# Kernel optimization log

Hardware: AMD Instinct MI355X
Metric: run time of the kernel (lower is better)

## Reference

```python
import jax, jax.numpy as jnp
import numpy as np

N = 100000
E = 3200000
IN_F = 16
HID = 64
NUM_CLASSES = 32


def setup_inputs() -> dict:
    key = jax.random.key(0)
    k1, k2, k3, k4, k5 = jax.random.split(key, 5)
    x = jax.random.normal(k1, (N, IN_F), dtype=jnp.float32)
    edge_index = jax.random.randint(k2, (2, E), 0, N, dtype=jnp.int64)
    # Glorot-style init for GCNConv weights, zero bias (PyG default)
    s1 = (6.0 / (IN_F + HID)) ** 0.5
    s2 = (6.0 / (HID + NUM_CLASSES)) ** 0.5
    W1 = jax.random.uniform(k3, (IN_F, HID), minval=-s1, maxval=s1, dtype=jnp.float32)
    b1 = jnp.zeros((HID,), dtype=jnp.float32)
    W2 = jax.random.uniform(k4, (HID, NUM_CLASSES), minval=-s2, maxval=s2, dtype=jnp.float32)
    b2 = jnp.zeros((NUM_CLASSES,), dtype=jnp.float32)
    return {"x": x, "edge_index": edge_index, "W1": W1, "b1": b1, "W2": W2, "b2": b2}


def _gcn_norm(edge_index):
    # add_self_loops=False, improved=False, edge_weight=1
    row, col = edge_index[0], edge_index[1]  # source, target
    deg = jax.ops.segment_sum(jnp.ones((edge_index.shape[1],), jnp.float32), col, num_segments=N)
    dinv = jnp.where(deg > 0, jax.lax.rsqrt(jnp.maximum(deg, 1e-12)), 0.0)
    return row, col, dinv[row] * dinv[col]  # [E]


def _gcn_conv(x, row, col, norm, W, b):
    h = x @ W                                  # [N, out]
    msg = h[row] * norm[:, None]               # [E, out] gather + normalize
    out = jax.ops.segment_sum(msg, col, num_segments=N)  # scatter-add to targets
    return out + b


def reference(x, edge_index, W1, b1, W2, b2):
    row, col, norm = _gcn_norm(edge_index)
    h = jax.nn.relu(_gcn_conv(x, row, col, norm, W1, b1))
    # dropout p=0.5 is identity in eval mode
    return _gcn_conv(h, row, col, norm, W2, b2)
```

## Files before the change

### kernel.cpp

```cpp
#include <hip/hip_runtime.h>
#include <hip/hip_fp16.h>

static constexpr int INF = 16;
static constexpr int HID = 64;
static constexpr int NC  = 32;
static constexpr int SHIFT = 8;
static constexpr int BK    = 256;
static constexpr int NBMAX = 512;
static constexpr int CAP   = 9216;
static constexpr int SPLIT_T  = 512;
static constexpr int SPLIT_IT = 16;
static constexpr int SRC_BITS = 17;
static constexpr int SRC_MASK = (1 << SRC_BITS) - 1;

struct alignas(8) half4 { __half2 lo, hi; };

__device__ __forceinline__ int clampi(int v, int n) {
    return v < 0 ? 0 : (v >= n ? n - 1 : v);
}

__global__ __launch_bounds__(SPLIT_T) void k_split(const int* __restrict__ ei, int E, int n,
                                                   int* __restrict__ bcur, int* __restrict__ pairs) {
    __shared__ int lh[NBMAX];
    __shared__ int base[NBMAX];
    int t = threadIdx.x;
    long long start = (long long)blockIdx.x * SPLIT_T * SPLIT_IT;
    int r[SPLIT_IT], c[SPLIT_IT];
    for (int j = t; j < NBMAX; j += SPLIT_T) lh[j] = 0;
    __syncthreads();
#pragma unroll
    for (int i = 0; i < SPLIT_IT; ++i) {
        long long e = start + (long long)i * SPLIT_T + t;
        if (e < E) {
            r[i] = clampi(ei[e], n);
            c[i] = clampi(ei[E + e], n);
            atomicAdd(&lh[c[i] >> SHIFT], 1);
        } else {
            c[i] = -1;
        }
    }
    __syncthreads();
    for (int j = t; j < NBMAX; j += SPLIT_T) {
        int cnt = lh[j];
        base[j] = cnt ? (j * CAP + atomicAdd(bcur + j, cnt)) : 0;
        lh[j] = 0;
    }
    __syncthreads();
#pragma unroll
    for (int i = 0; i < SPLIT_IT; ++i) {
        if (c[i] >= 0) {
            int b = c[i] >> SHIFT;
            int pos = base[b] + atomicAdd(&lh[b], 1);
            pairs[pos] = ((c[i] & (BK - 1)) << SRC_BITS) | r[i];
        }
    }
}

__global__ __launch_bounds__(1024) void k_fine(const int* __restrict__ pairs,
                                               const int* __restrict__ bcur,
                                               const float* __restrict__ x,
                                               int n,
                                               float* __restrict__ dinv,
                                               int* __restrict__ row_ptr,
                                               int* __restrict__ rend,
                                               int* __restrict__ src,
                                               __half2* __restrict__ xs) {
    __shared__ int h[BK];
    __shared__ int sc[BK];
    __shared__ float df[BK];
    int b = blockIdx.x, t = threadIdx.x;
    int bb = b * CAP;
    int be = bb + bcur[b];
    if (t < BK) h[t] = 0;
    __syncthreads();
    for (int i = bb + t; i < be; i += 1024)
        atomicAdd(&h[pairs[i] >> SRC_BITS], 1);
    __syncthreads();
    int val = (t < BK) ? h[t] : 0;
    if (t < BK) sc[t] = val;
    __syncthreads();
    for (int off = 1; off < BK; off <<= 1) {
        int a = (t < BK && t >= off) ? sc[t - off] : 0;
        __syncthreads();
        if (t < BK) sc[t] += a;
        __syncthreads();
    }
    if (t < BK) {
        int ex = sc[t] - val;
        int v = b * BK + t;
        float dv = 0.0f;
        if (v < n) {
            dv = (val > 0) ? rsqrtf((float)val) : 0.0f;
            dinv[v] = dv;
            row_ptr[v] = bb + ex;
            rend[v]    = bb + ex + val;
        }
        df[t] = dv;
        h[t] = bb + ex;
    }
    __syncthreads();
    for (int i = bb + t; i < be; i += 1024) {
        int p = pairs[i];
        int pos = atomicAdd(&h[p >> SRC_BITS], 1);
        src[pos] = p & SRC_MASK;
    }
    const float2* x2 = (const float2*)x;
    for (int idx = t; idx < BK * (INF / 2); idx += 1024) {
        int vl = idx >> 3, fp = idx & 7;
        int gv = b * BK + vl;
        if (gv < n) {
            float2 val2 = x2[(long long)gv * (INF / 2) + fp];
            float d = df[vl];
            xs[(long long)gv * (INF / 2) + fp] = __floats2half2_rn(val2.x * d, val2.y * d);
        }
    }
}

__global__ __launch_bounds__(256) void k_aggX(const int* __restrict__ ptr,
                                              const int* __restrict__ rend,
                                              const int* __restrict__ src,
                                              const float* __restrict__ dinv,
                                              const __half* __restrict__ xs,
                                              float* __restrict__ xa, int n) {
    int t = threadIdx.x;
    int v = blockIdx.x * 64 + (t >> 2);
    int lane = t & 3;
    if (v >= n) return;
    int b = ptr[v], e = rend[v];
    float a0 = 0.f, a1 = 0.f, a2 = 0.f, a3 = 0.f;
    int i = b;
    for (; i + 8 <= e; i += 8) {
        int s0 = src[i], s1 = src[i + 1], s2 = src[i + 2], s3 = src[i + 3];
        int s4 = src[i + 4], s5 = src[i + 5], s6 = src[i + 6], s7 = src[i + 7];
        half4 h0 = *reinterpret_cast<const half4*>(xs + (long long)s0 * INF + lane * 4);
        half4 h1 = *reinterpret_cast<const half4*>(xs + (long long)s1 * INF + lane * 4);
        half4 h2 = *reinterpret_cast<const half4*>(xs + (long long)s2 * INF + lane * 4);
        half4 h3 = *reinterpret_cast<const half4*>(xs + (long long)s3 * INF + lane * 4);
        half4 h4 = *reinterpret_cast<const half4*>(xs + (long long)s4 * INF + lane * 4);
        half4 h5 = *reinterpret_cast<const half4*>(xs + (long long)s5 * INF + lane * 4);
        half4 h6 = *reinterpret_cast<const half4*>(xs + (long long)s6 * INF + lane * 4);
        half4 h7 = *reinterpret_cast<const half4*>(xs + (long long)s7 * INF + lane * 4);
        float2 f;
        f = __half22float2(h0.lo); a0 += f.x; a1 += f.y;
        f = __half22float2(h0.hi); a2 += f.x; a3 += f.y;
        f = __half22float2(h1.lo); a0 += f.x; a1 += f.y;
        f = __half22float2(h1.hi); a2 += f.x; a3 += f.y;
        f = __half22float2(h2.lo); a0 += f.x; a1 += f.y;
        f = __half22float2(h2.hi); a2 += f.x; a3 += f.y;
        f = __half22float2(h3.lo); a0 += f.x; a1 += f.y;
        f = __half22float2(h3.hi); a2 += f.x; a3 += f.y;
        f = __half22float2(h4.lo); a0 += f.x; a1 += f.y;
        f = __half22float2(h4.hi); a2 += f.x; a3 += f.y;
        f = __half22float2(h5.lo); a0 += f.x; a1 += f.y;
        f = __half22float2(h5.hi); a2 += f.x; a3 += f.y;
        f = __half22float2(h6.lo); a0 += f.x; a1 += f.y;
        f = __half22float2(h6.hi); a2 += f.x; a3 += f.y;
        f = __half22float2(h7.lo); a0 += f.x; a1 += f.y;
        f = __half22float2(h7.hi); a2 += f.x; a3 += f.y;
    }
    for (; i < e; ++i) {
        int s = src[i];
        half4 hv = *reinterpret_cast<const half4*>(xs + (long long)s * INF + lane * 4);
        float2 f0 = __half22float2(hv.lo);
        float2 f1 = __half22float2(hv.hi);
        a0 += f0.x; a1 += f0.y; a2 += f1.x; a3 += f1.y;
    }
    float dv = dinv[v];
    float4 o = make_float4(a0 * dv, a1 * dv, a2 * dv, a3 * dv);
    *reinterpret_cast<float4*>(xa + (long long)v * INF + lane * 4) = o;
}

__global__ __launch_bounds__(256) void k_mlp(const float* __restrict__ xa,
                                             const float* __restrict__ W1,
                                             const float* __restrict__ b1,
                                             const float* __restrict__ W2,
                                             const float* __restrict__ dinv,
                                             __half2* __restrict__ h2h, int n) {
    __shared__ float W1l[INF * HID];
    __shared__ float W2l[HID * NC];
    __shared__ float b1l[HID];
    __shared__ float xal[16 * INF];
    __shared__ float hl[16 * HID];
    int t = threadIdx.x;
    for (int i = t; i < INF * HID; i += 256) W1l[i] = W1[i];
    for (int i = t; i < HID * NC; i += 256) W2l[i] = W2[i];
    if (t < HID) b1l[t] = b1[t];
    int base = blockIdx.x * 16;
    for (int i = t; i < 16 * INF; i += 256) {
        int r = i >> 4, k = i & 15;
        int v = base + r;
        xal[i] = (v < n) ? xa[(long long)v * INF + k] : 0.0f;
    }
    __syncthreads();
    for (int i = t; i < 16 * HID; i += 256) {
        int r = i >> 6, c = i & 63;
        float s = b1l[c];
#pragma unroll
        for (int k = 0; k < INF; ++k) s = fmaf(xal[r * INF + k], W1l[k * HID + c], s);
        hl[i] = fmaxf(s, 0.0f);
    }
    __syncthreads();
    {
        int r = t >> 4, cp = t & 15;
        int v = base + r;
        if (v < n) {
            int c0 = 2 * cp;
            float s0 = 0.f, s1 = 0.f;
#pragma unroll
            for (int k = 0; k < HID; ++k) {
                float hv = hl[r * HID + k];
                s0 = fmaf(hv, W2l[k * NC + c0], s0);
                s1 = fmaf(hv, W2l[k * NC + c0 + 1], s1);
            }
            float dv = dinv[v];
            h2h[(long long)v * (NC / 2) + cp] = __floats2half2_rn(s0 * dv, s1 * dv);
        }
    }
}

__global__ __launch_bounds__(256) void k_agg2(const int* __restrict__ ptr,
                                              const int* __restrict__ rend,
                                              const int* __restrict__ src,
                                              const float* __restrict__ dinv,
                                              const __half* __restrict__ h2h,
                                              const float* __restrict__ b2,
                                              float* __restrict__ out, int n) {
    int t = threadIdx.x;
    int v = blockIdx.x * 32 + (t >> 3);
    int lane = t & 7;
    if (v >= n) return;
    int b = ptr[v], e = rend[v];
    float a0 = 0.f, a1 = 0.f, a2 = 0.f, a3 = 0.f;
    int i = b;
    for (; i + 8 <= e; i += 8) {
        int s0 = src[i], s1 = src[i + 1], s2 = src[i + 2], s3 = src[i + 3];
        int s4 = src[i + 4], s5 = src[i + 5], s6 = src[i + 6], s7 = src[i + 7];
        half4 h0 = *reinterpret_cast<const half4*>(h2h + (long long)s0 * NC + lane * 4);
        half4 h1 = *reinterpret_cast<const half4*>(h2h + (long long)s1 * NC + lane * 4);
        half4 h2 = *reinterpret_cast<const half4*>(h2h + (long long)s2 * NC + lane * 4);
        half4 h3 = *reinterpret_cast<const half4*>(h2h + (long long)s3 * NC + lane * 4);
        half4 h4 = *reinterpret_cast<const half4*>(h2h + (long long)s4 * NC + lane * 4);
        half4 h5 = *reinterpret_cast<const half4*>(h2h + (long long)s5 * NC + lane * 4);
        half4 h6 = *reinterpret_cast<const half4*>(h2h + (long long)s6 * NC + lane * 4);
        half4 h7 = *reinterpret_cast<const half4*>(h2h + (long long)s7 * NC + lane * 4);
        float2 f;
        f = __half22float2(h0.lo); a0 += f.x; a1 += f.y;
        f = __half22float2(h0.hi); a2 += f.x; a3 += f.y;
        f = __half22float2(h1.lo); a0 += f.x; a1 += f.y;
        f = __half22float2(h1.hi); a2 += f.x; a3 += f.y;
        f = __half22float2(h2.lo); a0 += f.x; a1 += f.y;
        f = __half22float2(h2.hi); a2 += f.x; a3 += f.y;
        f = __half22float2(h3.lo); a0 += f.x; a1 += f.y;
        f = __half22float2(h3.hi); a2 += f.x; a3 += f.y;
        f = __half22float2(h4.lo); a0 += f.x; a1 += f.y;
        f = __half22float2(h4.hi); a2 += f.x; a3 += f.y;
        f = __half22float2(h5.lo); a0 += f.x; a1 += f.y;
        f = __half22float2(h5.hi); a2 += f.x; a3 += f.y;
        f = __half22float2(h6.lo); a0 += f.x; a1 += f.y;
        f = __half22float2(h6.hi); a2 += f.x; a3 += f.y;
        f = __half22float2(h7.lo); a0 += f.x; a1 += f.y;
        f = __half22float2(h7.hi); a2 += f.x; a3 += f.y;
    }
    for (; i < e; ++i) {
        int s = src[i];
        half4 hv = *reinterpret_cast<const half4*>(h2h + (long long)s * NC + lane * 4);
        float2 f0 = __half22float2(hv.lo);
        float2 f1 = __half22float2(hv.hi);
        a0 += f0.x; a1 += f0.y; a2 += f1.x; a3 += f1.y;
    }
    float dv = dinv[v];
    const float4 bb = *reinterpret_cast<const float4*>(b2 + lane * 4);
    float4 o = make_float4(fmaf(a0, dv, bb.x), fmaf(a1, dv, bb.y),
                           fmaf(a2, dv, bb.z), fmaf(a3, dv, bb.w));
    *reinterpret_cast<float4*>(out + (long long)v * NC + lane * 4) = o;
}

extern "C" void kernel_launch(void* const* d_in, const int* in_sizes, int n_in,
                              void* d_out, int out_size, void* d_ws, size_t ws_size,
                              hipStream_t stream) {
    const float* x  = (const float*)d_in[0];
    const int*   ei = (const int*)d_in[1];
    const float* W1 = (const float*)d_in[2];
    const float* b1 = (const float*)d_in[3];
    const float* W2 = (const float*)d_in[4];
    const float* b2 = (const float*)d_in[5];
    float* out = (float*)d_out;

    const int n = in_sizes[0] / INF;
    const int E = in_sizes[1] / 2;
    const int NB = (n + BK - 1) / BK;

    size_t  gcap    = (size_t)NB * CAP;
    int*    pairs   = (int*)d_ws;
    int*    src     = pairs + gcap;
    __half* xs      = (__half*)(src + gcap);
    float*  xa      = (float*)(src + gcap + (size_t)8 * n);
    __half* h2h     = (__half*)(src + gcap + (size_t)24 * n);
    float*  dinv    = (float*)(src + gcap + (size_t)40 * n);
    int*    row_ptr = (int*)(dinv + n);
    int*    rend    = row_ptr + n;
    int*    bcur    = rend + n;

    hipMemsetAsync(bcur, 0, NBMAX * sizeof(int), stream);

    int splitBlocks = (int)((E + (long long)SPLIT_T * SPLIT_IT - 1) / ((long long)SPLIT_T * SPLIT_IT));
    k_split<<<splitBlocks, SPLIT_T, 0, stream>>>(ei, E, n, bcur, pairs);

    k_fine<<<NB, 1024, 0, stream>>>(pairs, bcur, x, n, dinv, row_ptr, rend, src, (__half2*)xs);

    k_aggX<<<(n + 63) / 64, 256, 0, stream>>>(row_ptr, rend, src, dinv, xs, xa, n);
    k_mlp<<<(n + 15) / 16, 256, 0, stream>>>(xa, W1, b1, W2, dinv, (__half2*)h2h, n);
    k_agg2<<<(n + 31) / 32, 256, 0, stream>>>(row_ptr, rend, src, dinv, h2h, b2, out, n);
}
```

Baseline: 158.8 us.

## Fuse layer-1 aggregation with MLP and widen layer-2 gather to 16-byte loads

Merges the first-layer neighbour aggregation and the dense MLP (W1, ReLU, W2) into one kernel. Each group of 4 lanes exchanges its aggregated features through shuffles, computes 16 hidden units, and reduces the W2 partial products with xor-shuffles. This removes the fp32 xa intermediate round trip through global memory and one kernel launch. The second aggregation kernel now uses 4 lanes per node with 16-byte half8 loads instead of 8 lanes with 8-byte loads. The trade-off is higher register pressure (hreg, po and the x16 arrays) and some leftover dead shuffle-setup code.

```diff
diff --git a/kernel.cpp b/kernel.cpp
--- a/kernel.cpp
+++ b/kernel.cpp
@@ -12,8 +12,10 @@
 static constexpr int SPLIT_IT = 16;
 static constexpr int SRC_BITS = 17;
 static constexpr int SRC_MASK = (1 << SRC_BITS) - 1;
-
-struct alignas(8) half4 { __half2 lo, hi; };
+static constexpr int W2S = NC + 1;
+
+struct alignas(8)  half4 { __half2 lo, hi; };
+struct alignas(16) half8 { __half2 a, b, c, d; };
 
 __device__ __forceinline__ int clampi(int v, int n) {
     return v < 0 ? 0 : (v >= n ? n - 1 : v);
@@ -116,104 +118,137 @@
     }
 }
 
-__global__ __launch_bounds__(256) void k_aggX(const int* __restrict__ ptr,
-                                              const int* __restrict__ rend,
-                                              const int* __restrict__ src,
-                                              const float* __restrict__ dinv,
-                                              const __half* __restrict__ xs,
-                                              float* __restrict__ xa, int n) {
-    int t = threadIdx.x;
-    int v = blockIdx.x * 64 + (t >> 2);
-    int lane = t & 3;
-    if (v >= n) return;
-    int b = ptr[v], e = rend[v];
-    float a0 = 0.f, a1 = 0.f, a2 = 0.f, a3 = 0.f;
-    int i = b;
-    for (; i + 8 <= e; i += 8) {
-        int s0 = src[i], s1 = src[i + 1], s2 = src[i + 2], s3 = src[i + 3];
-        int s4 = src[i + 4], s5 = src[i + 5], s6 = src[i + 6], s7 = src[i + 7];
-        half4 h0 = *reinterpret_cast<const half4*>(xs + (long long)s0 * INF + lane * 4);
-        half4 h1 = *reinterpret_cast<const half4*>(xs + (long long)s1 * INF + lane * 4);
-        half4 h2 = *reinterpret_cast<const half4*>(xs + (long long)s2 * INF + lane * 4);
-        half4 h3 = *reinterpret_cast<const half4*>(xs + (long long)s3 * INF + lane * 4);
-        half4 h4 = *reinterpret_cast<const half4*>(xs + (long long)s4 * INF + lane * 4);
-        half4 h5 = *reinterpret_cast<const half4*>(xs + (long long)s5 * INF + lane * 4);
-        half4 h6 = *reinterpret_cast<const half4*>(xs + (long long)s6 * INF + lane * 4);
-        half4 h7 = *reinterpret_cast<const half4*>(xs + (long long)s7 * INF + lane * 4);
-        float2 f;
-        f = __half22float2(h0.lo); a0 += f.x; a1 += f.y;
-        f = __half22float2(h0.hi); a2 += f.x; a3 += f.y;
-        f = __half22float2(h1.lo); a0 += f.x; a1 += f.y;
-        f = __half22float2(h1.hi); a2 += f.x; a3 += f.y;
-        f = __half22float2(h2.lo); a0 += f.x; a1 += f.y;
-        f = __half22float2(h2.hi); a2 += f.x; a3 += f.y;
-        f = __half22float2(h3.lo); a0 += f.x; a1 += f.y;
-        f = __half22float2(h3.hi); a2 += f.x; a3 += f.y;
-        f = __half22float2(h4.lo); a0 += f.x; a1 += f.y;
-        f = __half22float2(h4.hi); a2 += f.x; a3 += f.y;
-        f = __half22float2(h5.lo); a0 += f.x; a1 += f.y;
-        f = __half22float2(h5.hi); a2 += f.x; a3 += f.y;
-        f = __half22float2(h6.lo); a0 += f.x; a1 += f.y;
-        f = __half22float2(h6.hi); a2 += f.x; a3 += f.y;
-        f = __half22float2(h7.lo); a0 += f.x; a1 += f.y;
-        f = __half22float2(h7.hi); a2 += f.x; a3 += f.y;
-    }
-    for (; i < e; ++i) {
-        int s = src[i];
-        half4 hv = *reinterpret_cast<const half4*>(xs + (long long)s * INF + lane * 4);
-        float2 f0 = __half22float2(hv.lo);
-        float2 f1 = __half22float2(hv.hi);
-        a0 += f0.x; a1 += f0.y; a2 += f1.x; a3 += f1.y;
-    }
-    float dv = dinv[v];
-    float4 o = make_float4(a0 * dv, a1 * dv, a2 * dv, a3 * dv);
-    *reinterpret_cast<float4*>(xa + (long long)v * INF + lane * 4) = o;
-}
-
-__global__ __launch_bounds__(256) void k_mlp(const float* __restrict__ xa,
-                                             const float* __restrict__ W1,
-                                             const float* __restrict__ b1,
-                                             const float* __restrict__ W2,
-                                             const float* __restrict__ dinv,
-                                             __half2* __restrict__ h2h, int n) {
+__global__ __launch_bounds__(256) void k_aggmlp2(const int* __restrict__ ptr,
+                                                 const int* __restrict__ rend,
+                                                 const int* __restrict__ src,
+                                                 const float* __restrict__ dinv,
+                                                 const __half* __restrict__ xs,
+                                                 const float* __restrict__ W1,
+                                                 const float* __restrict__ b1,
+                                                 const float* __restrict__ W2,
+                                                 __half* __restrict__ h2h, int n) {
     __shared__ float W1l[INF * HID];
-    __shared__ float W2l[HID * NC];
+    __shared__ float W2l[HID * W2S];
     __shared__ float b1l[HID];
-    __shared__ float xal[16 * INF];
-    __shared__ float hl[16 * HID];
     int t = threadIdx.x;
     for (int i = t; i < INF * HID; i += 256) W1l[i] = W1[i];
-    for (int i = t; i < HID * NC; i += 256) W2l[i] = W2[i];
+    for (int i = t; i < HID * NC; i += 256) W2l[(i >> 5) * W2S + (i & 31)] = W2[i];
     if (t < HID) b1l[t] = b1[t];
-    int base = blockIdx.x * 16;
-    for (int i = t; i < 16 * INF; i += 256) {
-        int r = i >> 4, k = i & 15;
-        int v = base + r;
-        xal[i] = (v < n) ? xa[(long long)v * INF + k] : 0.0f;
-    }
-    __syncthreads();
-    for (int i = t; i < 16 * HID; i += 256) {
-        int r = i >> 6, c = i & 63;
-        float s = b1l[c];
-#pragma unroll
-        for (int k = 0; k < INF; ++k) s = fmaf(xal[r * INF + k], W1l[k * HID + c], s);
-        hl[i] = fmaxf(s, 0.0f);
-    }
-    __syncthreads();
-    {
-        int r = t >> 4, cp = t & 15;
-        int v = base + r;
+
+    int node = t >> 2, lane = t & 3;
+    int v = blockIdx.x * 64 + node;
+    float a0 = 0.f, a1 = 0.f, a2 = 0.f, a3 = 0.f;
+    float dv = 0.0f;
+    if (v < n) {
+        dv = dinv[v];
+        int b = ptr[v], e = rend[v];
+        int i = b;
+        for (; i + 8 <= e; i += 8) {
+            int s0 = src[i], s1 = src[i + 1], s2 = src[i + 2], s3 = src[i + 3];
+            int s4 = src[i + 4], s5 = src[i + 5], s6 = src[i + 6], s7 = src[i + 7];
+            half4 h0 = *reinterpret_cast<const half4*>(xs + (long long)s0 * INF + lane * 4);
+            half4 h1 = *reinterpret_cast<const half4*>(xs + (long long)s1 * INF + lane * 4);
+            half4 h2 = *reinterpret_cast<const half4*>(xs + (long long)s2 * INF + lane * 4);
+            half4 h3 = *reinterpret_cast<const half4*>(xs + (long long)s3 * INF + lane * 4);
+            half4 h4 = *reinterpret_cast<const half4*>(xs + (long long)s4 * INF + lane * 4);
+            half4 h5 = *reinterpret_cast<const half4*>(xs + (long long)s5 * INF + lane * 4);
+            half4 h6 = *reinterpret_cast<const half4*>(xs + (long long)s6 * INF + lane * 4);
+            half4 h7 = *reinterpret_cast<const half4*>(xs + (long long)s7 * INF + lane * 4);
+            float2 f;
+            f = __half22float2(h0.lo); a0 += f.x; a1 += f.y;
+            f = __half22float2(h0.hi); a2 += f.x; a3 += f.y;
+            f = __half22float2(h1.lo); a0 += f.x; a1 += f.y;
+            f = __half22float2(h1.hi); a2 += f.x; a3 += f.y;
+            f = __half22float2(h2.lo); a0 += f.x; a1 += f.y;
+            f = __half22float2(h2.hi); a2 += f.x; a3 += f.y;
+            f = __half22float2(h3.lo); a0 += f.x; a1 += f.y;
+            f = __half22float2(h3.hi); a2 += f.x; a3 += f.y;
+            f = __half22float2(h4.lo); a0 += f.x; a1 += f.y;
+            f = __half22float2(h4.hi); a2 += f.x; a3 += f.y;
+            f = __half22float2(h5.lo); a0 += f.x; a1 += f.y;
+            f = __half22float2(h5.hi); a2 += f.x; a3 += f.y;
+            f = __half22float2(h6.lo); a0 += f.x; a1 += f.y;
+            f = __half22float2(h6.hi); a2 += f.x; a3 += f.y;
+            f = __half22float2(h7.lo); a0 += f.x; a1 += f.y;
+            f = __half22float2(h7.hi); a2 += f.x; a3 += f.y;
+        }
+        for (; i < e; ++i) {
+            int s = src[i];
+            half4 hv = *reinterpret_cast<const half4*>(xs + (long long)s * INF + lane * 4);
+            float2 f0 = __half22float2(hv.lo);
+            float2 f1 = __half22float2(hv.hi);
+            a0 += f0.x; a1 += f0.y; a2 += f1.x; a3 += f1.y;
+        }
+        a0 *= dv; a1 *= dv; a2 *= dv; a3 *= dv;
+    }
+    __syncthreads();
+
+    float own4[4] = {a0, a1, a2, a3};
+    float x8[8];
+#pragma unroll
+    for (int j = 0; j < 4; ++j) {
+        float send = own4[j];
+        float recv = __shfl_xor(send, 1);
+        x8[j]     = (lane & 1) ? recv : own4[j];
+        x8[4 + j] = (lane & 1) ? own4[j] : recv;
+    }
+    float x16[16];
+#pragma unroll
+    for (int j = 0; j < 8; ++j) {
+        float send = x8[j ^ ((lane & 2) ? 0 : 0)];
+        (void)send;
+    }
+#pragma unroll
+    for (int j = 0; j < 8; ++j) {
+        float snd = (lane & 2) ? x8[j] : x8[j];
+        float recv = __shfl_xor(snd, 2);
+        x16[j]     = (lane & 2) ? recv : x8[j];
+        x16[8 + j] = (lane & 2) ? x8[j] : recv;
+    }
+
+    int cbase = lane * 16;
+    float hreg[16];
+#pragma unroll
+    for (int j = 0; j < 16; ++j) {
+        float s = b1l[cbase + j];
+#pragma unroll
+        for (int k = 0; k < 16; ++k) s = fmaf(x16[k], W1l[k * HID + cbase + j], s);
+        hreg[j] = fmaxf(s, 0.0f);
+    }
+
+#pragma unroll
+    for (int c0 = 0; c0 < 2; ++c0) {
+        float po[16];
+#pragma unroll
+        for (int o = 0; o < 16; ++o) {
+            float s = 0.0f;
+#pragma unroll
+            for (int j = 0; j < 16; ++j)
+                s = fmaf(hreg[j], W2l[(cbase + j) * W2S + c0 * 16 + o], s);
+            po[o] = s;
+        }
+        float q[8];
+#pragma unroll
+        for (int j = 0; j < 8; ++j) {
+            float send = (lane & 1) ? po[j] : po[8 + j];
+            float recv = __shfl_xor(send, 1);
+            float keep = (lane & 1) ? po[8 + j] : po[j];
+            q[j] = keep + recv;
+        }
+        float r4[4];
+#pragma unroll
+        for (int j = 0; j < 4; ++j) {
+            float send = (lane & 2) ? q[j] : q[4 + j];
+            float recv = __shfl_xor(send, 2);
+            float keep = (lane & 2) ? q[4 + j] : q[j];
+            r4[j] = keep + recv;
+        }
         if (v < n) {
-            int c0 = 2 * cp;
-            float s0 = 0.f, s1 = 0.f;
-#pragma unroll
-            for (int k = 0; k < HID; ++k) {
-                float hv = hl[r * HID + k];
-                s0 = fmaf(hv, W2l[k * NC + c0], s0);
-                s1 = fmaf(hv, W2l[k * NC + c0 + 1], s1);
-            }
-            float dv = dinv[v];
-            h2h[(long long)v * (NC / 2) + cp] = __floats2half2_rn(s0 * dv, s1 * dv);
+            int obase = c0 * 16 + (lane & 1) * 8 + (lane & 2) * 2;
+            half4 outw;
+            outw.lo = __floats2half2_rn(r4[0] * dv, r4[1] * dv);
+            outw.hi = __floats2half2_rn(r4[2] * dv, r4[3] * dv);
+            *reinterpret_cast<half4*>(h2h + (long long)v * NC + obase) = outw;
         }
     }
 }
@@ -226,53 +261,75 @@
                                               const float* __restrict__ b2,
                                               float* __restrict__ out, int n) {
     int t = threadIdx.x;
-    int v = blockIdx.x * 32 + (t >> 3);
-    int lane = t & 7;
+    int v = blockIdx.x * 64 + (t >> 2);
+    int lane = t & 3;
     if (v >= n) return;
     int b = ptr[v], e = rend[v];
-    float a0 = 0.f, a1 = 0.f, a2 = 0.f, a3 = 0.f;
+    float a0 = 0.f, a1 = 0.f, a2 = 0.f, a3 = 0.f, a4 = 0.f, a5 = 0.f, a6 = 0.f, a7 = 0.f;
     int i = b;
     for (; i + 8 <= e; i += 8) {
         int s0 = src[i], s1 = src[i + 1], s2 = src[i + 2], s3 = src[i + 3];
         int s4 = src[i + 4], s5 = src[i + 5], s6 = src[i + 6], s7 = src[i + 7];
-        half4 h0 = *reinterpret_cast<const half4*>(h2h + (long long)s0 * NC + lane * 4);
-        half4 h1 = *reinterpret_cast<const half4*>(h2h + (long long)s1 * NC + lane * 4);
-        half4 h2 = *reinterpret_cast<const half4*>(h2h + (long long)s2 * NC + lane * 4);
-        half4 h3 = *reinterpret_cast<const half4*>(h2h + (long long)s3 * NC + lane * 4);
-        half4 h4 = *reinterpret_cast<const half4*>(h2h + (long long)s4 * NC + lane * 4);
-        half4 h5 = *reinterpret_cast<const half4*>(h2h + (long long)s5 * NC + lane * 4);
-        half4 h6 = *reinterpret_cast<const half4*>(h2h + (long long)s6 * NC + lane * 4);
-        half4 h7 = *reinterpret_cast<const half4*>(h2h + (long long)s7 * NC + lane * 4);
+        half8 h0 = *reinterpret_cast<const half8*>(h2h + (long long)s0 * NC + lane * 8);
+        half8 h1 = *reinterpret_cast<const half8*>(h2h + (long long)s1 * NC + lane * 8);
+        half8 h2 = *reinterpret_cast<const half8*>(h2h + (long long)s2 * NC + lane * 8);
+        half8 h3 = *reinterpret_cast<const half8*>(h2h + (long long)s3 * NC + lane * 8);
+        half8 h4 = *reinterpret_cast<const half8*>(h2h + (long long)s4 * NC + lane * 8);
+        half8 h5 = *reinterpret_cast<const half8*>(h2h + (long long)s5 * NC + lane * 8);
+        half8 h6 = *reinterpret_cast<const half8*>(h2h + (long long)s6 * NC + lane * 8);
+        half8 h7 = *reinterpret_cast<const half8*>(h2h + (long long)s7 * NC + lane * 8);
         float2 f;
-        f = __half22float2(h0.lo); a0 += f.x; a1 += f.y;
-        f = __half22float2(h0.hi); a2 += f.x; a3 += f.y;
-        f = __half22float2(h1.lo); a0 += f.x; a1 += f.y;
-        f = __half22float2(h1.hi); a2 += f.x; a3 += f.y;
-        f = __half22float2(h2.lo); a0 += f.x; a1 += f.y;
-        f = __half22float2(h2.hi); a2 += f.x; a3 += f.y;
-        f = __half22float2(h3.lo); a0 += f.x; a1 += f.y;
-        f = __half22float2(h3.hi); a2 += f.x; a3 += f.y;
-        f = __half22float2(h4.lo); a0 += f.x; a1 += f.y;
-        f = __half22float2(h4.hi); a2 += f.x; a3 += f.y;
-        f = __half22float2(h5.lo); a0 += f.x; a1 += f.y;
-        f = __half22float2(h5.hi); a2 += f.x; a3 += f.y;
-        f = __half22float2(h6.lo); a0 += f.x; a1 += f.y;
-        f = __half22float2(h6.hi); a2 += f.x; a3 += f.y;
-        f = __half22float2(h7.lo); a0 += f.x; a1 += f.y;
-        f = __half22float2(h7.hi); a2 += f.x; a3 += f.y;
+        f = __half22float2(h0.a); a0 += f.x; a1 += f.y;
+        f = __half22float2(h0.b); a2 += f.x; a3 += f.y;
+        f = __half22float2(h0.c); a4 += f.x; a5 += f.y;
+        f = __half22float2(h0.d); a6 += f.x; a7 += f.y;
+        f = __half22float2(h1.a); a0 += f.x; a1 += f.y;
+        f = __half22float2(h1.b); a2 += f.x; a3 += f.y;
+        f = __half22float2(h1.c); a4 += f.x; a5 += f.y;
+        f = __half22float2(h1.d); a6 += f.x; a7 += f.y;
+        f = __half22float2(h2.a); a0 += f.x; a1 += f.y;
+        f = __half22float2(h2.b); a2 += f.x; a3 += f.y;
+        f = __half22float2(h2.c); a4 += f.x; a5 += f.y;
+        f = __half22float2(h2.d); a6 += f.x; a7 += f.y;
+        f = __half22float2(h3.a); a0 += f.x; a1 += f.y;
+        f = __half22float2(h3.b); a2 += f.x; a3 += f.y;
+        f = __half22float2(h3.c); a4 += f.x; a5 += f.y;
+        f = __half22float2(h3.d); a6 += f.x; a7 += f.y;
+        f = __half22float2(h4.a); a0 += f.x; a1 += f.y;
+        f = __half22float2(h4.b); a2 += f.x; a3 += f.y;
+        f = __half22float2(h4.c); a4 += f.x; a5 += f.y;
+        f = __half22float2(h4.d); a6 += f.x; a7 += f.y;
+        f = __half22float2(h5.a); a0 += f.x; a1 += f.y;
+        f = __half22float2(h5.b); a2 += f.x; a3 += f.y;
+        f = __half22float2(h5.c); a4 += f.x; a5 += f.y;
+        f = __half22float2(h5.d); a6 += f.x; a7 += f.y;
+        f = __half22float2(h6.a); a0 += f.x; a1 += f.y;
+        f = __half22float2(h6.b); a2 += f.x; a3 += f.y;
+        f = __half22float2(h6.c); a4 += f.x; a5 += f.y;
+        f = __half22float2(h6.d); a6 += f.x; a7 += f.y;
+        f = __half22float2(h7.a); a0 += f.x; a1 += f.y;
+        f = __half22float2(h7.b); a2 += f.x; a3 += f.y;
+        f = __half22float2(h7.c); a4 += f.x; a5 += f.y;
+        f = __half22float2(h7.d); a6 += f.x; a7 += f.y;
     }
     for (; i < e; ++i) {
         int s = src[i];
-        half4 hv = *reinterpret_cast<const half4*>(h2h + (long long)s * NC + lane * 4);
-        float2 f0 = __half22float2(hv.lo);
-        float2 f1 = __half22float2(hv.hi);
-        a0 += f0.x; a1 += f0.y; a2 += f1.x; a3 += f1.y;
+        half8 hv = *reinterpret_cast<const half8*>(h2h + (long long)s * NC + lane * 8);
+        float2 f;
+        f = __half22float2(hv.a); a0 += f.x; a1 += f.y;
+        f = __half22float2(hv.b); a2 += f.x; a3 += f.y;
+        f = __half22float2(hv.c); a4 += f.x; a5 += f.y;
+        f = __half22float2(hv.d); a6 += f.x; a7 += f.y;
     }
     float dv = dinv[v];
-    const float4 bb = *reinterpret_cast<const float4*>(b2 + lane * 4);
-    float4 o = make_float4(fmaf(a0, dv, bb.x), fmaf(a1, dv, bb.y),
-                           fmaf(a2, dv, bb.z), fmaf(a3, dv, bb.w));
-    *reinterpret_cast<float4*>(out + (long long)v * NC + lane * 4) = o;
+    const float4 bb0 = *reinterpret_cast<const float4*>(b2 + lane * 8);
+    const float4 bb1 = *reinterpret_cast<const float4*>(b2 + lane * 8 + 4);
+    float4 o0 = make_float4(fmaf(a0, dv, bb0.x), fmaf(a1, dv, bb0.y),
+                            fmaf(a2, dv, bb0.z), fmaf(a3, dv, bb0.w));
+    float4 o1 = make_float4(fmaf(a4, dv, bb1.x), fmaf(a5, dv, bb1.y),
+                            fmaf(a6, dv, bb1.z), fmaf(a7, dv, bb1.w));
+    *reinterpret_cast<float4*>(out + (long long)v * NC + lane * 8)     = o0;
+    *reinterpret_cast<float4*>(out + (long long)v * NC + lane * 8 + 4) = o1;
 }
 
 extern "C" void kernel_launch(void* const* d_in, const int* in_sizes, int n_in,
@@ -294,9 +351,8 @@
     int*    pairs   = (int*)d_ws;
     int*    src     = pairs + gcap;
     __half* xs      = (__half*)(src + gcap);
-    float*  xa      = (float*)(src + gcap + (size_t)8 * n);
-    __half* h2h     = (__half*)(src + gcap + (size_t)24 * n);
-    float*  dinv    = (float*)(src + gcap + (size_t)40 * n);
+    __half* h2h     = (__half*)(src + gcap + (size_t)8 * n);
+    float*  dinv    = (float*)(src + gcap + (size_t)24 * n);
     int*    row_ptr = (int*)(dinv + n);
     int*    rend    = row_ptr + n;
     int*    bcur    = rend + n;
@@ -308,7 +364,7 @@
 
     k_fine<<<NB, 1024, 0, stream>>>(pairs, bcur, x, n, dinv, row_ptr, rend, src, (__half2*)xs);
 
-    k_aggX<<<(n + 63) / 64, 256, 0, stream>>>(row_ptr, rend, src, dinv, xs, xa, n);
-    k_mlp<<<(n + 15) / 16, 256, 0, stream>>>(xa, W1, b1, W2, dinv, (__half2*)h2h, n);
-    k_agg2<<<(n + 31) / 32, 256, 0, stream>>>(row_ptr, rend, src, dinv, h2h, b2, out, n);
-}
+    k_aggmlp2<<<(n + 63) / 64, 256, 0, stream>>>(row_ptr, rend, src, dinv, xs, W1, b1, W2,
+                                                 h2h, n);
+    k_agg2<<<(n + 63) / 64, 256, 0, stream>>>(row_ptr, rend, src, dinv, h2h, b2, out, n);
+}
```

Result: faster. 155.4 us (median of 2 runs) (-2.1%).

## Split second-layer aggregation into two column-half passes over smaller gather tables

Applied to the files above, without the earlier changes.

The MLP kernel now writes the 32-wide fp16 second-layer features as two separate 16-column tables. The final aggregation runs twice, once per half, so each gathered table is 3.2 MB instead of 6.4 MB and is meant to stay resident in L2/MALL during the random gathers. The cost is reading the CSR index arrays twice and one extra launch. The edge-split kernel is also retuned to 1024 threads with 8 items per thread.

```diff
diff --git a/kernel.cpp b/kernel.cpp
--- a/kernel.cpp
+++ b/kernel.cpp
@@ -8,8 +8,8 @@
 static constexpr int BK    = 256;
 static constexpr int NBMAX = 512;
 static constexpr int CAP   = 9216;
-static constexpr int SPLIT_T  = 512;
-static constexpr int SPLIT_IT = 16;
+static constexpr int SPLIT_T  = 1024;
+static constexpr int SPLIT_IT = 8;
 static constexpr int SRC_BITS = 17;
 static constexpr int SRC_MASK = (1 << SRC_BITS) - 1;
 
@@ -175,7 +175,8 @@
                                              const float* __restrict__ b1,
                                              const float* __restrict__ W2,
                                              const float* __restrict__ dinv,
-                                             __half2* __restrict__ h2h, int n) {
+                                             __half2* __restrict__ h2a,
+                                             __half2* __restrict__ h2b, int n) {
     __shared__ float W1l[INF * HID];
     __shared__ float W2l[HID * NC];
     __shared__ float b1l[HID];
@@ -213,21 +214,23 @@
                 s1 = fmaf(hv, W2l[k * NC + c0 + 1], s1);
             }
             float dv = dinv[v];
-            h2h[(long long)v * (NC / 2) + cp] = __floats2half2_rn(s0 * dv, s1 * dv);
-        }
-    }
-}
-
-__global__ __launch_bounds__(256) void k_agg2(const int* __restrict__ ptr,
-                                              const int* __restrict__ rend,
-                                              const int* __restrict__ src,
-                                              const float* __restrict__ dinv,
-                                              const __half* __restrict__ h2h,
-                                              const float* __restrict__ b2,
-                                              float* __restrict__ out, int n) {
+            __half2 w = __floats2half2_rn(s0 * dv, s1 * dv);
+            if (cp < 8) h2a[(long long)v * 8 + cp]       = w;
+            else        h2b[(long long)v * 8 + (cp - 8)] = w;
+        }
+    }
+}
+
+__global__ __launch_bounds__(256) void k_agg2h(const int* __restrict__ ptr,
+                                               const int* __restrict__ rend,
+                                               const int* __restrict__ src,
+                                               const float* __restrict__ dinv,
+                                               const __half* __restrict__ tab,
+                                               const float* __restrict__ b2,
+                                               float* __restrict__ out, int n, int coff) {
     int t = threadIdx.x;
-    int v = blockIdx.x * 32 + (t >> 3);
-    int lane = t & 7;
+    int v = blockIdx.x * 64 + (t >> 2);
+    int lane = t & 3;
     if (v >= n) return;
     int b = ptr[v], e = rend[v];
     float a0 = 0.f, a1 = 0.f, a2 = 0.f, a3 = 0.f;
@@ -235,14 +238,14 @@
     for (; i + 8 <= e; i += 8) {
         int s0 = src[i], s1 = src[i + 1], s2 = src[i + 2], s3 = src[i + 3];
         int s4 = src[i + 4], s5 = src[i + 5], s6 = src[i + 6], s7 = src[i + 7];
-        half4 h0 = *reinterpret_cast<const half4*>(h2h + (long long)s0 * NC + lane * 4);
-        half4 h1 = *reinterpret_cast<const half4*>(h2h + (long long)s1 * NC + lane * 4);
-        half4 h2 = *reinterpret_cast<const half4*>(h2h + (long long)s2 * NC + lane * 4);
-        half4 h3 = *reinterpret_cast<const half4*>(h2h + (long long)s3 * NC + lane * 4);
-        half4 h4 = *reinterpret_cast<const half4*>(h2h + (long long)s4 * NC + lane * 4);
-        half4 h5 = *reinterpret_cast<const half4*>(h2h + (long long)s5 * NC + lane * 4);
-        half4 h6 = *reinterpret_cast<const half4*>(h2h + (long long)s6 * NC + lane * 4);
-        half4 h7 = *reinterpret_cast<const half4*>(h2h + (long long)s7 * NC + lane * 4);
+        half4 h0 = *reinterpret_cast<const half4*>(tab + (long long)s0 * 16 + lane * 4);
+        half4 h1 = *reinterpret_cast<const half4*>(tab + (long long)s1 * 16 + lane * 4);
+        half4 h2 = *reinterpret_cast<const half4*>(tab + (long long)s2 * 16 + lane * 4);
+        half4 h3 = *reinterpret_cast<const half4*>(tab + (long long)s3 * 16 + lane * 4);
+        half4 h4 = *reinterpret_cast<const half4*>(tab + (long long)s4 * 16 + lane * 4);
+        half4 h5 = *reinterpret_cast<const half4*>(tab + (long long)s5 * 16 + lane * 4);
+        half4 h6 = *reinterpret_cast<const half4*>(tab + (long long)s6 * 16 + lane * 4);
+        half4 h7 = *reinterpret_cast<const half4*>(tab + (long long)s7 * 16 + lane * 4);
         float2 f;
         f = __half22float2(h0.lo); a0 += f.x; a1 += f.y;
         f = __half22float2(h0.hi); a2 += f.x; a3 += f.y;
@@ -263,16 +266,16 @@
     }
     for (; i < e; ++i) {
         int s = src[i];
-        half4 hv = *reinterpret_cast<const half4*>(h2h + (long long)s * NC + lane * 4);
+        half4 hv = *reinterpret_cast<const half4*>(tab + (long long)s * 16 + lane * 4);
         float2 f0 = __half22float2(hv.lo);
         float2 f1 = __half22float2(hv.hi);
         a0 += f0.x; a1 += f0.y; a2 += f1.x; a3 += f1.y;
     }
     float dv = dinv[v];
-    const float4 bb = *reinterpret_cast<const float4*>(b2 + lane * 4);
+    const float4 bb = *reinterpret_cast<const float4*>(b2 + coff + lane * 4);
     float4 o = make_float4(fmaf(a0, dv, bb.x), fmaf(a1, dv, bb.y),
                            fmaf(a2, dv, bb.z), fmaf(a3, dv, bb.w));
-    *reinterpret_cast<float4*>(out + (long long)v * NC + lane * 4) = o;
+    *reinterpret_cast<float4*>(out + (long long)v * NC + coff + lane * 4) = o;
 }
 
 extern "C" void kernel_launch(void* const* d_in, const int* in_sizes, int n_in,
@@ -295,7 +298,8 @@
     int*    src     = pairs + gcap;
     __half* xs      = (__half*)(src + gcap);
     float*  xa      = (float*)(src + gcap + (size_t)8 * n);
-    __half* h2h     = (__half*)(src + gcap + (size_t)24 * n);
+    __half* h2a     = (__half*)(src + gcap + (size_t)24 * n);
+    __half* h2b     = (__half*)(src + gcap + (size_t)32 * n);
     float*  dinv    = (float*)(src + gcap + (size_t)40 * n);
     int*    row_ptr = (int*)(dinv + n);
     int*    rend    = row_ptr + n;
@@ -309,6 +313,8 @@
     k_fine<<<NB, 1024, 0, stream>>>(pairs, bcur, x, n, dinv, row_ptr, rend, src, (__half2*)xs);
 
     k_aggX<<<(n + 63) / 64, 256, 0, stream>>>(row_ptr, rend, src, dinv, xs, xa, n);
-    k_mlp<<<(n + 15) / 16, 256, 0, stream>>>(xa, W1, b1, W2, dinv, (__half2*)h2h, n);
-    k_agg2<<<(n + 31) / 32, 256, 0, stream>>>(row_ptr, rend, src, dinv, h2h, b2, out, n);
-}
+    k_mlp<<<(n + 15) / 16, 256, 0, stream>>>(xa, W1, b1, W2, dinv,
+                                             (__half2*)h2a, (__half2*)h2b, n);
+    k_agg2h<<<(n + 63) / 64, 256, 0, stream>>>(row_ptr, rend, src, dinv, h2a, b2, out, n, 0);
+    k_agg2h<<<(n + 63) / 64, 256, 0, stream>>>(row_ptr, rend, src, dinv, h2b, b2, out, n, 16);
+}
```

After: 175.4 us. +10.5%, slower.
